# Kernel tuning notes

Measured on AMD Instinct MI355X. Metric: run time of the kernel, lower is better.

Reference implementation:

```python
import jax, jax.numpy as jnp
import numpy as np

T, B, F, P = 1024, 2048, 11, 256
KAPPA_MAX = 0.1
N_GRID = 100


def setup_inputs() -> dict:
    key = jax.random.key(0)
    k1, k2, k3, k4, k5 = jax.random.split(key, 5)
    aidx = jax.random.randint(k1, (T, B), 0, 2)
    actions = jax.nn.one_hot(aidx, 2, dtype=jnp.float32)            # (T,B,2) one-hot choice
    rewards = jax.random.bernoulli(k2, 0.5, (T, B, 2)).astype(jnp.float32)
    cd_cur = jax.random.uniform(k3, (T, B, 1), minval=-0.1, maxval=0.1)
    cd_next = jax.random.uniform(k4, (T, B, 1), minval=-0.1, maxval=0.1)
    meta = jnp.zeros((T, B, 4), dtype=jnp.float32)                  # timestep/trial/block/experiment (unused)
    pid = jax.random.randint(k5, (B,), 0, P).astype(jnp.float32)
    pid_feat = jnp.broadcast_to(pid[None, :, None], (T, B, 1))
    inputs = jnp.concatenate([actions, rewards, cd_cur, cd_next, meta, pid_feat], axis=-1)
    inputs = inputs[:, None]                                        # (T, 1, B, 11)
    return {
        "inputs": inputs,
        "beta_raw": jnp.zeros((P,), dtype=jnp.float32),
        "sigma_raw": jnp.zeros((P,), dtype=jnp.float32),
    }


def reference(inputs, beta_raw, sigma_raw):
    p_mu = jnp.linspace(0.0, 1.0, N_GRID)                           # (100,)
    x = jnp.nan_to_num(inputs[:, 0])                                # (T, B, 11)
    pid = x[0, :, -1].astype(jnp.int32)                             # (B,)
    beta = jnp.clip(jax.nn.softplus(beta_raw) + 1.0, 1.0, 25.0)[pid]    # (B,)
    sigma = jnp.clip(jax.nn.sigmoid(sigma_raw) * 0.09 + 0.01, 0.01, 0.1)[pid]  # (B,)
    inv_s = 1.0 / (sigma * jnp.sqrt(2.0))

    def ncdf(v, mean):
        return 0.5 * (1.0 + jax.lax.erf((v - mean) * inv_s))

    def state_beliefs(cd):
        u = ncdf(0.0, cd)
        v = ncdf(-KAPPA_MAX, cd)
        w = ncdf(KAPPA_MAX, cd)
        denom = jnp.maximum(w - v, 1e-10)
        pi_0 = jnp.clip((u - v) / denom, 0.0, 1.0)
        pi_1 = jnp.clip((w - u) / denom, 0.0, 1.0)
        return pi_0, pi_1

    def step(belief, x_t):
        acts = x_t[:, :2]
        rews = x_t[:, 2:4]
        cd_current = x_t[:, 4]
        cd_next = x_t[:, 5]
        had_choice = acts.sum(-1) > 0
        action_idx = jnp.argmax(acts, axis=-1)
        reward_scalar = (rews * acts).sum(-1)
        pi_0, pi_1 = state_beliefs(cd_current)
        r = jnp.where(action_idx == 0, reward_scalar, 1.0 - reward_scalar)
        q_0 = pi_1 * r + pi_0 * (1.0 - r)
        q_1 = (2.0 * r - 1.0) * (pi_0 - pi_1)
        update = q_1[:, None] * p_mu + q_0[:, None]                 # (B, 100)
        update = jnp.where(had_choice[:, None], update, 1.0)
        belief = jnp.maximum(belief * update, 1e-30)
        belief_norm = belief / belief.sum(-1, keepdims=True)
        E_mu = (belief_norm * p_mu).sum(-1)                         # (B,)
        pi_0n, pi_1n = state_beliefs(cd_next)
        v_a0 = (pi_0n - pi_1n) * E_mu + pi_1n
        v_a1 = (pi_1n - pi_0n) * E_mu + pi_0n
        logits_t = beta[:, None] * jnp.stack([v_a0, v_a1], axis=-1)  # (B, 2)
        return belief, logits_t

    belief0 = jnp.ones((x.shape[1], N_GRID), dtype=x.dtype)
    belief, logits = jax.lax.scan(step, belief0, x)                 # logits: (T, B, 2)
    logits = logits[:, None]                                        # (T, 1, B, 2)
    return logits, belief
```

## Files before the change

### kernel.cpp

```cpp
#include <hip/hip_runtime.h>
#include <math.h>

#define TT  1024
#define BB  2048
#define FF  11
#define PP  256
#define NG  100
#define NCH 32
#define LCH (TT / NCH)
#define JJ  4

typedef float f32x2 __attribute__((ext_vector_type(2)));

__device__ __forceinline__ float nz(float v) { return (v != v) ? 0.f : v; }

__device__ __forceinline__ float erf_fast(float x) {
    float ax = fabsf(x);
    float t  = __builtin_amdgcn_rcpf(fmaf(0.3275911f, ax, 1.f));
    float y  = fmaf(fmaf(fmaf(fmaf(1.061405429f, t, -1.453152027f), t,
                              1.421413741f), t, -0.284496736f), t, 0.254829592f);
    y *= t;
    float r = fmaf(-y, __expf(-ax * ax), 1.f);
    return copysignf(r, x);
}

__device__ __forceinline__ float4 q_from_rec(
    float a0, float a1, float r0, float r1, float cdc, float cdn,
    float beta, float inv_s)
{
    float u = 0.5f * (1.f + erf_fast((0.0f  - cdc) * inv_s));
    float v = 0.5f * (1.f + erf_fast((-0.1f - cdc) * inv_s));
    float w = 0.5f * (1.f + erf_fast((0.1f  - cdc) * inv_s));
    float inv = 1.f / fmaxf(w - v, 1e-10f);
    float pi0 = fminf(fmaxf((u - v) * inv, 0.f), 1.f);
    float pi1 = fminf(fmaxf((w - u) * inv, 0.f), 1.f);

    u = 0.5f * (1.f + erf_fast((0.0f  - cdn) * inv_s));
    v = 0.5f * (1.f + erf_fast((-0.1f - cdn) * inv_s));
    w = 0.5f * (1.f + erf_fast((0.1f  - cdn) * inv_s));
    inv = 1.f / fmaxf(w - v, 1e-10f);
    float pi0n = fminf(fmaxf((u - v) * inv, 0.f), 1.f);
    float pi1n = fminf(fmaxf((w - u) * inv, 0.f), 1.f);

    float rs = r0 * a0 + r1 * a1;
    float r  = (a0 >= a1) ? rs : 1.f - rs;
    float q0 = pi1 * r + pi0 * (1.f - r);
    float q1 = (2.f * r - 1.f) * (pi0 - pi1);
    if (!((a0 + a1) > 0.f)) { q0 = 1.f; q1 = 0.f; }
    return make_float4(q0, q1, beta * pi1n, beta * pi0n);
}


__global__ __launch_bounds__(256) void phaseAq_kernel(
    const float* __restrict__ x, const float* __restrict__ beta_raw,
    const float* __restrict__ sigma_raw, float4* __restrict__ QC,
    float* __restrict__ UC)
{
    __shared__ float  sx[4][LCH * 88];
    __shared__ float2 sq[4][64];
    const int lane = threadIdx.x & 63;
    const int wib  = threadIdx.x >> 6;
    const int W    = blockIdx.x * 4 + wib;
    const int wg   = W & 255;
    const int c    = W >> 8;
    const int g    = lane & 7;
    const int sl   = lane >> 3;
    const int b    = wg * 8 + g;
    const int t0   = c * LCH;
    float*  sxw = sx[wib];
    float2* sqw = sq[wib];

    {
        const float4* x4 = (const float4*)x;
        float4* s4 = (float4*)sxw;
        #pragma unroll
        for (int j = 0; j < 11; ++j) {
            int idx = lane + 64 * j;
            int row = idx / 22;
            int col = idx - row * 22;
            s4[idx] = x4[(size_t)(t0 + row) * 5632 + wg * 22 + col];
        }
    }

    int pid = (int)nz(x[(size_t)b * FF + 10]);
    pid = pid < 0 ? 0 : (pid > PP - 1 ? PP - 1 : pid);
    float br = beta_raw[pid];
    float sr = sigma_raw[pid];
    float sp   = fmaxf(br, 0.f) + log1pf(__expf(-fabsf(br)));
    float beta = fminf(fmaxf(sp + 1.f, 1.f), 25.f);
    float sig  = fminf(fmaxf(__builtin_amdgcn_rcpf(1.f + __expf(-sr)) * 0.09f + 0.01f,
                             0.01f), 0.1f);
    float inv_s = 1.f / (sig * 1.41421356237309505f);

    f32x2 p[7];
    #pragma unroll
    for (int k = 0; k < 7; ++k)
        p[k] = (f32x2){ (float)(sl + 16 * k)     * (1.f / 99.f),
                        (float)(sl + 16 * k + 8) * (1.f / 99.f) };

    f32x2 U[7];
    #pragma unroll
    for (int k = 0; k < 7; ++k) U[k] = (f32x2){1.f, 1.f};

    __syncthreads();

    for (int tt = 0; tt < LCH; tt += 8) {
        const float* rec = sxw + (tt + sl) * 88 + g * 11;
        float a0 = nz(rec[0]), a1 = nz(rec[1]), r0 = nz(rec[2]),
              r1 = nz(rec[3]), dc = nz(rec[4]), dn = nz(rec[5]);
        float4 qc = q_from_rec(a0, a1, r0, r1, dc, dn, beta, inv_s);
        QC[(size_t)(t0 + tt + sl) * BB + b] = qc;

        sqw[sl * 8 + g] = make_float2(qc.x, qc.y);
        __builtin_amdgcn_wave_barrier();
        #pragma unroll
        for (int j = 0; j < 8; ++j) {
            float2 qj = sqw[j * 8 + g];
            f32x2 qx = { qj.x, qj.x }, qy = { qj.y, qj.y };
            #pragma unroll
            for (int k = 0; k < 7; ++k) {
                f32x2 u = qy * p[k] + qx;
                U[k] *= u;
            }
        }
        __builtin_amdgcn_wave_barrier();
    }

    float* dst = UC + (size_t)c * (NG * BB) + b;
    #pragma unroll
    for (int k = 0; k < 6; ++k) {
        dst[(size_t)(sl + 16 * k) * BB]     = U[k].x;
        dst[(size_t)(sl + 16 * k + 8) * BB] = U[k].y;
    }
    if (sl < 4) dst[(size_t)(sl + 96) * BB] = U[6].x;
}

__global__ __launch_bounds__(256) void phaseB_kernel(
    const float* __restrict__ UC, float* __restrict__ BE)
{
    const int flat = blockIdx.x * 256 + threadIdx.x;
    float be = 1.f;
    #pragma unroll
    for (int c = 0; c < NCH; ++c) {
        BE[(size_t)c * (BB * NG) + flat] = be;
        float u = UC[(size_t)c * (BB * NG) + flat];
        be = fmaxf(be * u, 1e-30f);
    }
}

__global__ __launch_bounds__(256) void phaseC_kernel(
    const float4* __restrict__ QC, const float* __restrict__ BE,
    float* __restrict__ out)
{
    const int lane = threadIdx.x & 63;
    const int wib  = threadIdx.x >> 6;
    const int W    = blockIdx.x * 4 + wib;
    const int wg   = W & 255;
    const int c    = W >> 8;
    const int sl   = lane & 7;
    const int g    = lane >> 3;
    const int b    = wg * 8 + g;
    const int t0   = c * LCH;

    f32x2 p[7];
    #pragma unroll
    for (int k = 0; k < 7; ++k)
        p[k] = (f32x2){ (float)(sl + 16 * k)     * (1.f / 99.f),
                        (float)(sl + 16 * k + 8) * (1.f / 99.f) };
    const f32x2 clA = { 1e-30f, 1e-30f };
    const f32x2 cl6 = { (sl < 4) ? 1e-30f : 0.f, 0.f };

    const float* ebase = BE + (size_t)c * (BB * NG) + b;
    f32x2 be[7];
    #pragma unroll
    for (int k = 0; k < 6; ++k)
        be[k] = (f32x2){ ebase[(size_t)(sl + 16 * k) * BB],
                         ebase[(size_t)(sl + 16 * k + 8) * BB] };
    be[6] = (f32x2){ (sl < 4) ? ebase[(size_t)(sl + 96) * BB] : 0.f, 0.f };

    const char* QCb = (const char*)QC;
    char* outb = (char*)out;
    unsigned off  = ((unsigned)t0 * BB + (unsigned)b) * 16u;
    unsigned soff = ((unsigned)t0 * (2 * BB) + 2 * (unsigned)b) * 4u;

    float4 pre[JJ];
    #pragma unroll
    for (int j = 0; j < JJ; ++j)
        pre[j] = *(const float4*)(QCb + (off + (unsigned)j * (BB * 16u)));
    off += JJ * (BB * 16u);

    for (int tt = 0; tt < LCH; tt += JJ) {
        float S[JJ], Sp[JJ], Zv[JJ], Wv[JJ];
        #pragma unroll
        for (int j = 0; j < JJ; ++j) {
            float4 q = pre[j];
            pre[j] = *(const float4*)(QCb + (off + (unsigned)j * (BB * 16u)));
            f32x2 qx = { q.x, q.x }, qy = { q.y, q.y };
            #pragma unroll
            for (int k = 0; k < 7; ++k) {
                f32x2 u = qy * p[k] + qx;
                be[k] = __builtin_elementwise_max(be[k] * u,
                                                  (k == 6) ? cl6 : clA);
            }
            f32x2 sA = ((be[0] + be[1]) + (be[2] + be[3]))
                     + ((be[4] + be[5]) + be[6]);
            S[j] = sA.x + sA.y;
            f32x2 a1 = be[0] * p[0], a2 = be[1] * p[1];
            a1 = be[2] * p[2] + a1;  a2 = be[3] * p[3] + a2;
            a1 = be[4] * p[4] + a1;  a2 = be[5] * p[5] + a2;
            a1 = be[6] * p[6] + a1;
            f32x2 aa = a1 + a2;
            Sp[j] = aa.x + aa.y;
            Zv[j] = q.z;
            Wv[j] = q.w;
        }
        off += JJ * (BB * 16u);
        #pragma unroll
        for (int j = 0; j < JJ; ++j) {
            float st = S[j], sr = Sp[j];
            {
                int t;
                t = __builtin_amdgcn_update_dpp(0, __float_as_int(st), 0xB1, 0xF, 0xF, true);
                st += __int_as_float(t);
                t = __builtin_amdgcn_update_dpp(0, __float_as_int(sr), 0xB1, 0xF, 0xF, true);
                sr += __int_as_float(t);
                t = __builtin_amdgcn_update_dpp(0, __float_as_int(st), 0x4E, 0xF, 0xF, true);
                st += __int_as_float(t);
                t = __builtin_amdgcn_update_dpp(0, __float_as_int(sr), 0x4E, 0xF, 0xF, true);
                sr += __int_as_float(t);
                t = __builtin_amdgcn_update_dpp(0, __float_as_int(st), 0x141, 0xF, 0xF, true);
                st += __int_as_float(t);
                t = __builtin_amdgcn_update_dpp(0, __float_as_int(sr), 0x141, 0xF, 0xF, true);
                sr += __int_as_float(t);
            }
            float E  = sr * __builtin_amdgcn_rcpf(st);
            float A  = Wv[j] - Zv[j];
            float l0 = fmaf(A, E, Zv[j]);
            float l1 = fmaf(-A, E, Wv[j]);
            if (sl == 0)
                *(float2*)(outb + (soff + (unsigned)j * (2 * BB * 4u))) =
                    make_float2(l0, l1);
        }
        soff += JJ * (2 * BB * 4u);
    }

    if (c == NCH - 1) {
        float* bel = out + (size_t)TT * BB * 2 + (size_t)b * NG;
        #pragma unroll
        for (int k = 0; k < 6; ++k) {
            bel[sl + 16 * k]     = be[k].x;
            bel[sl + 16 * k + 8] = be[k].y;
        }
        if (sl < 4) bel[sl + 96] = be[6].x;
    }
}

extern "C" void kernel_launch(void* const* d_in, const int* in_sizes, int n_in,
                              void* d_out, int out_size, void* d_ws, size_t ws_size,
                              hipStream_t stream)
{
    const float* x         = (const float*)d_in[0];
    const float* beta_raw  = (const float*)d_in[1];
    const float* sigma_raw = (const float*)d_in[2];
    float* out = (float*)d_out;

    char* ws = (char*)d_ws;
    float4* QC = (float4*)ws;
    float*  UC = (float*)(ws + (size_t)TT * BB * 16);
    float*  BE = (float*)(ws + (size_t)TT * BB * 16 + (size_t)NCH * BB * NG * 4);

    phaseAq_kernel<<<(BB / 8) * NCH / 4, 256, 0, stream>>>(x, beta_raw, sigma_raw, QC, UC);
    phaseB_kernel<<<(BB * NG) / 256, 256, 0, stream>>>(UC, BE);
    phaseC_kernel<<<(BB / 8) * NCH / 4, 256, 0, stream>>>(QC, BE, out);
}
```

Measured before the change: 192.5 us.

## Stream input tiles through registers with prefetch instead of bulk LDS staging

Phase-A input staging changes from loading a whole 32-step chunk into shared memory up front to a register double-buffered prefetch of 8-step tiles. This shrinks LDS per block and overlaps the next tile's global loads with compute on the current one. Launch bounds now request 6 blocks per CU to raise occupancy, which may cap registers and risk spills. The LDS buffer is only written and read within each wave, so wave barriers are used in place of the block barrier.

```diff
diff --git a/kernel.cpp b/kernel.cpp
--- a/kernel.cpp
+++ b/kernel.cpp
@@ -51,12 +51,12 @@
 }
 
 
-__global__ __launch_bounds__(256) void phaseAq_kernel(
+__global__ __launch_bounds__(256, 6) void phaseAq_kernel(
     const float* __restrict__ x, const float* __restrict__ beta_raw,
     const float* __restrict__ sigma_raw, float4* __restrict__ QC,
     float* __restrict__ UC)
 {
-    __shared__ float  sx[4][LCH * 88];
+    __shared__ float  sx[4][8 * 88];
     __shared__ float2 sq[4][64];
     const int lane = threadIdx.x & 63;
     const int wib  = threadIdx.x >> 6;
@@ -70,17 +70,16 @@
     float*  sxw = sx[wib];
     float2* sqw = sq[wib];
 
-    {
-        const float4* x4 = (const float4*)x;
-        float4* s4 = (float4*)sxw;
-        #pragma unroll
-        for (int j = 0; j < 11; ++j) {
-            int idx = lane + 64 * j;
-            int row = idx / 22;
-            int col = idx - row * 22;
-            s4[idx] = x4[(size_t)(t0 + row) * 5632 + wg * 22 + col];
-        }
-    }
+    const int r0i = lane / 22,         c0i = lane - r0i * 22;
+    const int r1i = (lane + 64) / 22,  c1i = (lane + 64) - r1i * 22;
+    const int r2i = (lane + 128) / 22, c2i = (lane + 128) - r2i * 22;
+    const float4* x4 = (const float4*)x;
+    const size_t base = (size_t)t0 * 5632 + (size_t)wg * 22;
+
+    float4 pf0 = x4[base + (size_t)r0i * 5632 + c0i];
+    float4 pf1 = x4[base + (size_t)r1i * 5632 + c1i];
+    float4 pf2;
+    if (lane < 48) pf2 = x4[base + (size_t)r2i * 5632 + c2i];
 
     int pid = (int)nz(x[(size_t)b * FF + 10]);
     pid = pid < 0 ? 0 : (pid > PP - 1 ? PP - 1 : pid);
@@ -102,14 +101,24 @@
     #pragma unroll
     for (int k = 0; k < 7; ++k) U[k] = (f32x2){1.f, 1.f};
 
-    __syncthreads();
-
-    for (int tt = 0; tt < LCH; tt += 8) {
-        const float* rec = sxw + (tt + sl) * 88 + g * 11;
+    float4* s4 = (float4*)sxw;
+    #pragma unroll
+    for (int tb = 0; tb < 4; ++tb) {
+        s4[lane]      = pf0;
+        s4[lane + 64] = pf1;
+        if (lane < 48) s4[lane + 128] = pf2;
+        __builtin_amdgcn_wave_barrier();
+        if (tb < 3) {
+            const size_t nb = base + (size_t)((tb + 1) * 8) * 5632;
+            pf0 = x4[nb + (size_t)r0i * 5632 + c0i];
+            pf1 = x4[nb + (size_t)r1i * 5632 + c1i];
+            if (lane < 48) pf2 = x4[nb + (size_t)r2i * 5632 + c2i];
+        }
+        const float* rec = sxw + sl * 88 + g * 11;
         float a0 = nz(rec[0]), a1 = nz(rec[1]), r0 = nz(rec[2]),
               r1 = nz(rec[3]), dc = nz(rec[4]), dn = nz(rec[5]);
         float4 qc = q_from_rec(a0, a1, r0, r1, dc, dn, beta, inv_s);
-        QC[(size_t)(t0 + tt + sl) * BB + b] = qc;
+        QC[(size_t)(t0 + tb * 8 + sl) * BB + b] = qc;
 
         sqw[sl * 8 + g] = make_float2(qc.x, qc.y);
         __builtin_amdgcn_wave_barrier();
```

After: 197.3 us. 1.02x slower.
